# Kernel optimization log

Measured on AMD Instinct MI355X. Metric: run time of the kernel, lower is better.

The kernel has to match this reference:

```python
import math
import jax, jax.numpy as jnp
import numpy as np

T_LEN, BATCH = 215, 256
D_INP = 36; D_MODEL = 36          # d_model must be 36 for internal dims to be consistent
D_T = D_MODEL + 36                # 72: transformer encoder width
N_HEAD = 4; D_HEAD = D_T // N_HEAD
D_FF = 128; N_LAYERS = 2; D_STATIC = 9; N_CLASSES = 2
N_NODES = 36

def _layer_norm(x, g, b, eps=1e-5):
    mu = jnp.mean(x, -1, keepdims=True)
    var = jnp.mean((x - mu) ** 2, -1, keepdims=True)
    return (x - mu) / jnp.sqrt(var + eps) * g + b

def _forward(src, static, times, lengths, W_enc, b_enc, W_emb, b_emb, Wq, bq, Wk, bk, Wv, bv, Wskip, bskip, enc_in_w, enc_in_b, enc_out_w, enc_out_b, enc_ff1_w, enc_ff1_b, enc_ff2_w, enc_ff2_b, enc_ln1_g, enc_ln1_b, enc_ln2_g, enc_ln2_b, mlp_w1, mlp_b1, mlp_w2, mlp_b2):
    T, B = src.shape[0], src.shape[1]
    x = (src[:, :, :D_INP] @ W_enc.T + b_enc) * math.sqrt(D_MODEL)          # [T,B,36]
    # positional encoding: 18 timescales = max_len ** linspace(0,1,18)
    timescales = jnp.asarray(215.0 ** np.linspace(0.0, 1.0, D_MODEL // 2), jnp.float32)
    scaled = times[:, :, None] / timescales                                  # [T,B,18]
    pe = jnp.concatenate([jnp.sin(scaled), jnp.cos(scaled)], -1)             # [T,B,36]
    emb = static @ W_emb.T + b_emb                                           # [B,36]
    mask = jnp.arange(T)[None, :] >= lengths[:, None]                        # [B,T] True = pad
    # --- batched TransformerConv over fully-connected 36-node graph (replaces per-sample loop) ---
    q = x @ Wq.T + bq; k = x @ Wk.T + bk; v = x @ Wv.T + bv
    skip = x @ Wskip.T + bskip
    scores = jnp.einsum('ibe,jbe->bij', q[:N_NODES], k[:N_NODES]) / math.sqrt(36.0)  # i=tgt, j=src
    A = jax.nn.softmax(scores, -1)                      # per-target softmax over incoming edges
    msg = jnp.einsum('bij,jbe->ibe', A, v[:N_NODES])    # edge_weights are all ones
    gout = skip.at[:N_NODES].add(msg)                   # [T,B,36]; rows >= 36 have no in-edges
    # per-edge alpha flattened in nonzero(adj) order: e = src*36 + tgt
    alpha_all = A.transpose(0, 2, 1).reshape(B, N_NODES * N_NODES).T         # [1296,B]
    sq = jnp.sum(alpha_all ** 2, 0)
    d2 = jnp.maximum(sq[:, None] + sq[None, :] - 2.0 * (alpha_all.T @ alpha_all), 0.0)
    distance = jnp.mean(jnp.sqrt(jnp.where(d2 > 0, d2, 1.0)) * (d2 > 0))     # mean pairwise L2
    # --- 2-layer post-norm transformer encoder, width 72, key padding mask ---
    h = jnp.concatenate([gout, pe], -1)                                      # [T,B,72]
    neg = jnp.where(mask[:, None, None, :], -1e9, 0.0)                       # [B,1,1,T]
    for l in range(N_LAYERS):
        qkv = h @ enc_in_w[l].T + enc_in_b[l]
        qh, kh, vh = [t.reshape(T, B, N_HEAD, D_HEAD) for t in jnp.split(qkv, 3, -1)]
        s = jnp.einsum('tbhd,sbhd->bhts', qh, kh) / math.sqrt(D_HEAD) + neg
        ctx = jnp.einsum('bhts,sbhd->tbhd', jax.nn.softmax(s, -1), vh).reshape(T, B, D_T)
        h = _layer_norm(h + ctx @ enc_out_w[l].T + enc_out_b[l], enc_ln1_g[l], enc_ln1_b[l])
        ff = jax.nn.relu(h @ enc_ff1_w[l].T + enc_ff1_b[l]) @ enc_ff2_w[l].T + enc_ff2_b[l]
        h = _layer_norm(h + ff, enc_ln2_g[l], enc_ln2_b[l])
    # masked mean over time, denominator lengths+1 (as in original)
    valid = (~mask).astype(h.dtype).T[:, :, None]                            # [T,B,1]
    pooled = jnp.sum(h * valid, 0) / (lengths.astype(h.dtype)[:, None] + 1.0)
    feat = jnp.concatenate([pooled, emb], -1)                                # [B,108]
    logits = jax.nn.relu(feat @ mlp_w1.T + mlp_b1) @ mlp_w2.T + mlp_b2
    return logits, distance

def setup_inputs() -> dict:
    key = jax.random.key(0)
    ks = jax.random.split(key, 40)
    def nrm(i, shape, s=0.05):
        return jax.random.normal(ks[i], shape, jnp.float32) * s
    return {
        'src': jax.random.normal(ks[0], (T_LEN, BATCH, 2 * D_INP), jnp.float32),
        'static': jax.random.normal(ks[1], (BATCH, D_STATIC), jnp.float32),
        'times': jnp.tile(jnp.arange(T_LEN, dtype=jnp.float32)[:, None], (1, BATCH)),
        'lengths': jax.random.randint(ks[2], (BATCH,), 1, T_LEN + 1),
        'W_enc': nrm(3, (D_MODEL, D_INP)), 'b_enc': jnp.zeros((D_MODEL,), jnp.float32),
        'W_emb': nrm(4, (D_MODEL, D_STATIC)), 'b_emb': jnp.zeros((D_MODEL,), jnp.float32),
        'Wq': nrm(5, (36, 36)), 'bq': nrm(6, (36,)),
        'Wk': nrm(7, (36, 36)), 'bk': nrm(8, (36,)),
        'Wv': nrm(9, (36, 36)), 'bv': nrm(10, (36,)),
        'Wskip': nrm(11, (36, 36)), 'bskip': nrm(12, (36,)),
        'enc_in_w': nrm(13, (N_LAYERS, 3 * D_T, D_T)), 'enc_in_b': nrm(14, (N_LAYERS, 3 * D_T)),
        'enc_out_w': nrm(15, (N_LAYERS, D_T, D_T)), 'enc_out_b': nrm(16, (N_LAYERS, D_T)),
        'enc_ff1_w': nrm(17, (N_LAYERS, D_FF, D_T)), 'enc_ff1_b': nrm(18, (N_LAYERS, D_FF)),
        'enc_ff2_w': nrm(19, (N_LAYERS, D_T, D_FF)), 'enc_ff2_b': nrm(20, (N_LAYERS, D_T)),
        'enc_ln1_g': jnp.ones((N_LAYERS, D_T), jnp.float32), 'enc_ln1_b': jnp.zeros((N_LAYERS, D_T), jnp.float32),
        'enc_ln2_g': jnp.ones((N_LAYERS, D_T), jnp.float32), 'enc_ln2_b': jnp.zeros((N_LAYERS, D_T), jnp.float32),
        'mlp_w1': nrm(21, (108, 108)), 'mlp_b1': nrm(22, (108,)),
        'mlp_w2': nrm(23, (N_CLASSES, 108)), 'mlp_b2': nrm(24, (N_CLASSES,)),
    }

def reference(src, static, times, lengths, W_enc, b_enc, W_emb, b_emb, Wq, bq, Wk, bk, Wv, bv, Wskip, bskip, enc_in_w, enc_in_b, enc_out_w, enc_out_b, enc_ff1_w, enc_ff1_b, enc_ff2_w, enc_ff2_b, enc_ln1_g, enc_ln1_b, enc_ln2_g, enc_ln2_b, mlp_w1, mlp_b1, mlp_w2, mlp_b2):
    return _forward(src, static, times, lengths, W_enc, b_enc, W_emb, b_emb, Wq, bq, Wk, bk, Wv, bv, Wskip, bskip, enc_in_w, enc_in_b, enc_out_w, enc_out_b, enc_ff1_w, enc_ff1_b, enc_ff2_w, enc_ff2_b, enc_ln1_g, enc_ln1_b, enc_ln2_g, enc_ln2_b, mlp_w1, mlp_b1, mlp_w2, mlp_b2)
```

## Files before the change

kernel.cpp:

```cpp
#include <hip/hip_runtime.h>

#define TT 215
#define BB 256
#define ROWS (TT * BB)

typedef __attribute__((ext_vector_type(8))) short short8;
typedef __attribute__((ext_vector_type(4))) float f32x4;

__device__ __forceinline__ unsigned short f2bf_rn(float x) {
    unsigned int u = __float_as_uint(x);
    u = u + 0x7FFFu + ((u >> 16) & 1u);
    return (unsigned short)(u >> 16);
}
__device__ __forceinline__ float bf2f(unsigned short b) {
    return __uint_as_float(((unsigned int)b) << 16);
}

__global__ void k_prep(const float* __restrict__ enc_in_w, const float* __restrict__ ff1_w,
                       const float* __restrict__ ff2_w, const float* __restrict__ enc_out_w,
                       unsigned short* __restrict__ Whi, unsigned short* __restrict__ Wlo,
                       unsigned short* __restrict__ F1hi, unsigned short* __restrict__ F1lo,
                       unsigned short* __restrict__ F2hi, unsigned short* __restrict__ F2lo,
                       unsigned short* __restrict__ Ohi, unsigned short* __restrict__ Olo,
                       float* __restrict__ ts) {
    int g = blockIdx.x * 256 + threadIdx.x;
    if (g < 18) ts[g] = (float)pow(215.0, (double)g / 17.0);
    if (g < 2 * 216 * 96) {
        int l = g / (216 * 96), rem = g % (216 * 96);
        int o = rem / 96, k = rem % 96;
        float v = (k < 72) ? enc_in_w[((size_t)l * 216 + o) * 72 + k] : 0.f;
        unsigned short hi = f2bf_rn(v);
        Whi[g] = hi; Wlo[g] = f2bf_rn(v - bf2f(hi));
    }
    if (g < 2 * 128 * 96) {
        int l = g / (128 * 96), rem = g % (128 * 96);
        int j = rem / 96, k = rem % 96;
        float v = (k < 72) ? ff1_w[((size_t)l * 128 + j) * 72 + k] : 0.f;
        unsigned short hi = f2bf_rn(v);
        F1hi[g] = hi; F1lo[g] = f2bf_rn(v - bf2f(hi));
    }
    if (g < 2 * 72 * 128) {
        float v = ff2_w[g];
        unsigned short hi = f2bf_rn(v);
        F2hi[g] = hi; F2lo[g] = f2bf_rn(v - bf2f(hi));
    }
    if (g < 2 * 72 * 96) {
        int l = g / (72 * 96), rem = g % (72 * 96);
        int o = rem / 96, k = rem % 96;
        float v = (k < 72) ? enc_out_w[((size_t)l * 72 + o) * 72 + k] : 0.f;
        unsigned short hi = f2bf_rn(v);
        Ohi[g] = hi; Olo[g] = f2bf_rn(v - bf2f(hi));
    }
}

__global__ __launch_bounds__(256, 1) void k_enc1(const float* __restrict__ src,
                                                 const float* __restrict__ W,
                                                 const float* __restrict__ bias,
                                                 float* __restrict__ x) {
    int row = blockIdx.x * 256 + threadIdx.x;
    int o0 = blockIdx.y * 9;
    float s[36];
    const float4* sv = (const float4*)(src + (size_t)row * 72);
#pragma unroll
    for (int k = 0; k < 9; ++k) {
        float4 v = sv[k];
        s[4 * k] = v.x; s[4 * k + 1] = v.y; s[4 * k + 2] = v.z; s[4 * k + 3] = v.w;
    }
    float* xp = x + (size_t)row * 36 + o0;
#pragma unroll
    for (int o = 0; o < 9; ++o) {
        float a = bias[o0 + o];
        const float* w = W + (size_t)(o0 + o) * 36;
#pragma unroll
        for (int i = 0; i < 36; ++i) a = fmaf(s[i], w[i], a);
        xp[o] = a * 6.0f;
    }
}

__global__ __launch_bounds__(256, 1) void k_enc2(const float* __restrict__ x,
                                                 const float* __restrict__ W,
                                                 const float* __restrict__ bias,
                                                 float* __restrict__ h) {
    int row = blockIdx.x * 256 + threadIdx.x;
    int o0 = blockIdx.y * 9;
    float xr[36];
    const float4* xv = (const float4*)(x + (size_t)row * 36);
#pragma unroll
    for (int k = 0; k < 9; ++k) {
        float4 v = xv[k];
        xr[4 * k] = v.x; xr[4 * k + 1] = v.y; xr[4 * k + 2] = v.z; xr[4 * k + 3] = v.w;
    }
    float* hp = h + (size_t)row * 72 + o0;
#pragma unroll
    for (int o = 0; o < 9; ++o) {
        float a = bias[o0 + o];
        const float* w = W + (size_t)(o0 + o) * 36;
#pragma unroll
        for (int i = 0; i < 36; ++i) a = fmaf(xr[i], w[i], a);
        hp[o] = a;
    }
}

__global__ __launch_bounds__(256) void k_pe(const float* __restrict__ times,
                                            const float* __restrict__ ts,
                                            float* __restrict__ h) {
    int idx = blockIdx.x * 256 + threadIdx.x;
    int d = idx % 36, row = idx / 36;
    float t = times[row];
    float val;
    if (d < 18) val = sinf(t / ts[d]);
    else        val = cosf(t / ts[d - 18]);
    h[(size_t)row * 72 + 36 + d] = val;
}

__global__ __launch_bounds__(256, 1) void k_graph_qkv(const float* __restrict__ x,
                                                      const float* __restrict__ Wq, const float* __restrict__ bq,
                                                      const float* __restrict__ Wk, const float* __restrict__ bk,
                                                      const float* __restrict__ Wv, const float* __restrict__ bv,
                                                      float* __restrict__ qg, float* __restrict__ kg,
                                                      float* __restrict__ vg) {
    int row = blockIdx.x * 256 + threadIdx.x;
    int mat = blockIdx.y >> 2;
    int o0 = (blockIdx.y & 3) * 9;
    const float* W; const float* bias; float* out;
    if (mat == 0)      { W = Wq; bias = bq; out = qg; }
    else if (mat == 1) { W = Wk; bias = bk; out = kg; }
    else               { W = Wv; bias = bv; out = vg; }
    float xr[36];
    const float4* xv = (const float4*)(x + (size_t)row * 36);
#pragma unroll
    for (int k = 0; k < 9; ++k) {
        float4 v = xv[k];
        xr[4 * k] = v.x; xr[4 * k + 1] = v.y; xr[4 * k + 2] = v.z; xr[4 * k + 3] = v.w;
    }
    float* op = out + (size_t)row * 36 + o0;
#pragma unroll
    for (int o = 0; o < 9; ++o) {
        float a = bias[o0 + o];
        const float* w = W + (size_t)(o0 + o) * 36;
#pragma unroll
        for (int i = 0; i < 36; ++i) a = fmaf(xr[i], w[i], a);
        op[o] = a;
    }
}

__global__ void k_graph_attn(const float* __restrict__ qg, const float* __restrict__ kg,
                             const float* __restrict__ vg, float* __restrict__ h,
                             float* __restrict__ Abuf, float* __restrict__ sqv) {
    __shared__ float q[1296], k[1296], v[1296], A[1296];
    __shared__ float red[128];
    int b = blockIdx.x, tid = threadIdx.x;
    for (int i = tid; i < 1296; i += 128) {
        int t = i / 36, e = i % 36;
        int g = (t * BB + b) * 36 + e;
        q[i] = qg[g]; k[i] = kg[g]; v[i] = vg[g];
    }
    __syncthreads();
    for (int i = tid; i < 1296; i += 128) {
        int r = i / 36, c = i % 36;
        float a = 0.f;
#pragma unroll
        for (int e = 0; e < 36; ++e) a = fmaf(q[r * 36 + e], k[c * 36 + e], a);
        A[i] = a * (1.0f / 6.0f);
    }
    __syncthreads();
    if (tid < 36) {
        float m = -1e30f;
        for (int j = 0; j < 36; ++j) m = fmaxf(m, A[tid * 36 + j]);
        float s = 0.f;
        for (int j = 0; j < 36; ++j) { float e = expf(A[tid * 36 + j] - m); A[tid * 36 + j] = e; s += e; }
        float inv = 1.0f / s;
        for (int j = 0; j < 36; ++j) A[tid * 36 + j] *= inv;
    }
    __syncthreads();
    float lsq = 0.f;
    for (int i = tid; i < 1296; i += 128) {
        float a = A[i];
        Abuf[(size_t)b * 1296 + i] = a;
        lsq = fmaf(a, a, lsq);
        int r = i / 36, e = i % 36;
        float m = 0.f;
#pragma unroll
        for (int j = 0; j < 36; ++j) m = fmaf(A[r * 36 + j], v[j * 36 + e], m);
        h[((size_t)r * BB + b) * 72 + e] += m;
    }
    red[tid] = lsq;
    __syncthreads();
    for (int s = 64; s > 0; s >>= 1) { if (tid < s) red[tid] += red[tid + s]; __syncthreads(); }
    if (tid == 0) sqv[b] = red[0];
}

__global__ void k_gram(const float* __restrict__ Abuf, const float* __restrict__ sqv,
                       float* __restrict__ rowsum) {
    __shared__ float Arow[1296];
    __shared__ float red[256];
    int b1 = blockIdx.x, tid = threadIdx.x;
    for (int i = tid; i < 1296; i += 256) Arow[i] = Abuf[(size_t)b1 * 1296 + i];
    __syncthreads();
    int b2 = tid;
    const float* a2 = Abuf + (size_t)b2 * 1296;
    float dot = 0.f;
    for (int e = 0; e < 1296; ++e) dot = fmaf(Arow[e], a2[e], dot);
    float d2 = fmaxf(sqv[b1] + sqv[b2] - 2.0f * dot, 0.0f);
    red[tid] = (d2 > 0.0f) ? sqrtf(d2) : 0.0f;
    __syncthreads();
    for (int s = 128; s > 0; s >>= 1) { if (tid < s) red[tid] += red[tid + s]; __syncthreads(); }
    if (tid == 0) rowsum[b1] = red[0];
}

__global__ __launch_bounds__(256, 1) void k_qkv(const float* __restrict__ h,
                                                const unsigned short* __restrict__ Whi,
                                                const unsigned short* __restrict__ Wlo,
                                                const float* __restrict__ bias,
                                                float* __restrict__ qkv) {
    int tid = threadIdx.x;
    int w = tid >> 6;
    int lane = tid & 63;
    int n16 = lane & 15;
    int quad = lane >> 4;
    int m0 = blockIdx.x * 64 + w * 16;
    int r = m0 + n16;
    short8 Ahi[3], Alo[3];
#pragma unroll
    for (int s = 0; s < 3; ++s) {
        int k0 = s * 32 + quad * 8;
        float v[8];
        if (k0 < 72) {
            const float4* ap = (const float4*)(h + (size_t)r * 72 + k0);
            float4 v0 = ap[0], v1 = ap[1];
            v[0] = v0.x; v[1] = v0.y; v[2] = v0.z; v[3] = v0.w;
            v[4] = v1.x; v[5] = v1.y; v[6] = v1.z; v[7] = v1.w;
        } else {
#pragma unroll
            for (int j = 0; j < 8; ++j) v[j] = 0.f;
        }
        short8 ph, pl;
#pragma unroll
        for (int j = 0; j < 8; ++j) {
            unsigned short hi = f2bf_rn(v[j]);
            ph[j] = (short)hi;
            pl[j] = (short)f2bf_rn(v[j] - bf2f(hi));
        }
        Ahi[s] = ph; Alo[s] = pl;
    }
    f32x4 acc[14];
#pragma unroll
    for (int t = 0; t < 14; ++t) acc[t] = (f32x4){0.f, 0.f, 0.f, 0.f};
#pragma unroll
    for (int t = 0; t < 14; ++t) {
        int o = t * 16 + n16;
        int oc = (o > 215) ? 215 : o;
        const short8* bh = (const short8*)(Whi + (size_t)oc * 96);
        const short8* bl = (const short8*)(Wlo + (size_t)oc * 96);
        f32x4 a = acc[t];
#pragma unroll
        for (int s = 0; s < 3; ++s) {
            short8 Bh = bh[s * 4 + quad];
            short8 Bl = bl[s * 4 + quad];
            a = __builtin_amdgcn_mfma_f32_16x16x32_bf16(Ahi[s], Bh, a, 0, 0, 0);
            a = __builtin_amdgcn_mfma_f32_16x16x32_bf16(Ahi[s], Bl, a, 0, 0, 0);
            a = __builtin_amdgcn_mfma_f32_16x16x32_bf16(Alo[s], Bh, a, 0, 0, 0);
        }
        acc[t] = a;
    }
#pragma unroll
    for (int t = 0; t < 14; ++t) {
        int col = t * 16 + n16;
        if (col < 216) {
            float b = bias[col];
#pragma unroll
            for (int reg = 0; reg < 4; ++reg) {
                int row = m0 + quad * 4 + reg;
                qkv[(size_t)row * 216 + col] = acc[t][reg] + b;
            }
        }
    }
}

__global__ __launch_bounds__(256, 1) void k_attn(const float* __restrict__ qkv,
                                                 const int* __restrict__ lengths,
                                                 float* __restrict__ ctx) {
    __shared__ __attribute__((aligned(16))) unsigned short Kb[215 * 40];
    __shared__ __attribute__((aligned(16))) unsigned short Vt[32 * 232];
    __shared__ __attribute__((aligned(16))) unsigned short Pw[4][16 * 232];
    int b = blockIdx.x & (BB - 1);
    int hh = blockIdx.x >> 8;
    int tid = threadIdx.x;
    int len = lengths[b];
    for (int i = tid; i < (215 * 40) / 2; i += 256) ((unsigned int*)Kb)[i] = 0u;
    for (int i = tid; i < (32 * 232) / 2; i += 256) ((unsigned int*)Vt)[i] = 0u;
    __syncthreads();
    for (int i = tid; i < len * 18; i += 256) {
        int s = i / 18, d = i % 18;
        size_t base2 = ((size_t)s * BB + b) * 216 + hh * 18 + d;
        Kb[s * 40 + d] = f2bf_rn(qkv[base2 + 72]);
        Vt[d * 232 + s] = f2bf_rn(qkv[base2 + 144]);
    }
    __syncthreads();
    int w = tid >> 6;
    int lane = tid & 63;
    int n16 = lane & 15;
    int quad = lane >> 4;
    const float scale = 0.23570226039551587f;
    int nk2 = (len + 31) >> 5;
    int nkt = nk2 * 2;
    int nstrips = (len + 15) >> 4;
    unsigned short* P = &Pw[w][0];
    for (int strip = w; strip < nstrips; strip += 4) {
        int q0 = strip * 16;
        int qr = q0 + n16; if (qr > 214) qr = 214;
        float qv[8];
#pragma unroll
        for (int j = 0; j < 8; ++j) qv[j] = 0.f;
        {
            const float* qp = qkv + ((size_t)qr * BB + b) * 216 + hh * 18;
            int d0 = quad * 8;
            if (d0 < 16) {
                const float2* q2 = (const float2*)(qp + d0);
                float2 a0 = q2[0], a1 = q2[1], a2 = q2[2], a3 = q2[3];
                qv[0] = a0.x; qv[1] = a0.y; qv[2] = a1.x; qv[3] = a1.y;
                qv[4] = a2.x; qv[5] = a2.y; qv[6] = a3.x; qv[7] = a3.y;
            } else if (d0 == 16) {
                qv[0] = qp[16]; qv[1] = qp[17];
            }
        }
        short8 Qhi, Qlo;
#pragma unroll
        for (int j = 0; j < 8; ++j) {
            float v = qv[j] * scale;
            unsigned short hi = f2bf_rn(v);
            Qhi[j] = (short)hi;
            Qlo[j] = (short)f2bf_rn(v - bf2f(hi));
        }
        float lsum[4] = {0.f, 0.f, 0.f, 0.f};
        for (int kt = 0; kt < nkt; ++kt) {
            int key = kt * 16 + n16;
            int kr = (key > 214) ? 214 : key;
            short8 Bk = *(const short8*)(Kb + kr * 40 + quad * 8);
            f32x4 S = (f32x4){0.f, 0.f, 0.f, 0.f};
            S = __builtin_amdgcn_mfma_f32_16x16x32_bf16(Qlo, Bk, S, 0, 0, 0);
            S = __builtin_amdgcn_mfma_f32_16x16x32_bf16(Qhi, Bk, S, 0, 0, 0);
#pragma unroll
            for (int reg = 0; reg < 4; ++reg) {
                float p = (key < len) ? __expf(S[reg]) : 0.f;
                lsum[reg] += p;
                P[(quad * 4 + reg) * 232 + kt * 16 + n16] = f2bf_rn(p);
            }
        }
#pragma unroll
        for (int m = 1; m < 16; m <<= 1) {
#pragma unroll
            for (int reg = 0; reg < 4; ++reg) lsum[reg] += __shfl_xor(lsum[reg], m);
        }
        f32x4 o0 = (f32x4){0.f, 0.f, 0.f, 0.f};
        f32x4 o1 = (f32x4){0.f, 0.f, 0.f, 0.f};
        for (int k2 = 0; k2 < nk2; ++k2) {
            short8 Af = *(const short8*)(P + n16 * 232 + k2 * 32 + quad * 8);
            short8 Bv0 = *(const short8*)(Vt + n16 * 232 + k2 * 32 + quad * 8);
            short8 Bv1 = *(const short8*)(Vt + (16 + n16) * 232 + k2 * 32 + quad * 8);
            o0 = __builtin_amdgcn_mfma_f32_16x16x32_bf16(Af, Bv0, o0, 0, 0, 0);
            o1 = __builtin_amdgcn_mfma_f32_16x16x32_bf16(Af, Bv1, o1, 0, 0, 0);
        }
#pragma unroll
        for (int reg = 0; reg < 4; ++reg) {
            int t = q0 + quad * 4 + reg;
            if (t < len) {
                float inv = 1.0f / lsum[reg];
                float* cb = ctx + ((size_t)t * BB + b) * 72 + hh * 18;
                cb[n16] = o0[reg] * inv;
                if (n16 < 2) cb[16 + n16] = o1[reg] * inv;
            }
        }
    }
}

__global__ __launch_bounds__(256, 1) void k_outln(const float* __restrict__ ctx,
                                                  const unsigned short* __restrict__ Ohi,
                                                  const unsigned short* __restrict__ Olo,
                                                  const float* __restrict__ bias,
                                                  const float* __restrict__ g,
                                                  const float* __restrict__ beta,
                                                  float* __restrict__ h) {
    int tid = threadIdx.x;
    int w = tid >> 6;
    int lane = tid & 63;
    int n16 = lane & 15;
    int quad = lane >> 4;
    int m0 = blockIdx.x * 64 + w * 16;
    int r = m0 + n16;
    short8 Ahi[3], Alo[3];
#pragma unroll
    for (int s = 0; s < 3; ++s) {
        int k0 = s * 32 + quad * 8;
        float v[8];
        if (k0 < 72) {
            const float4* ap = (const float4*)(ctx + (size_t)r * 72 + k0);
            float4 v0 = ap[0], v1 = ap[1];
            v[0] = v0.x; v[1] = v0.y; v[2] = v0.z; v[3] = v0.w;
            v[4] = v1.x; v[5] = v1.y; v[6] = v1.z; v[7] = v1.w;
        } else {
#pragma unroll
            for (int j = 0; j < 8; ++j) v[j] = 0.f;
        }
        short8 ph, pl;
#pragma unroll
        for (int j = 0; j < 8; ++j) {
            unsigned short hi = f2bf_rn(v[j]);
            ph[j] = (short)hi;
            pl[j] = (short)f2bf_rn(v[j] - bf2f(hi));
        }
        Ahi[s] = ph; Alo[s] = pl;
    }
    f32x4 acc[5];
#pragma unroll
    for (int t = 0; t < 5; ++t) acc[t] = (f32x4){0.f, 0.f, 0.f, 0.f};
#pragma unroll
    for (int t = 0; t < 5; ++t) {
        int o = t * 16 + n16;
        int oc = (o > 71) ? 71 : o;
        const short8* bh = (const short8*)(Ohi + (size_t)oc * 96);
        const short8* bl = (const short8*)(Olo + (size_t)oc * 96);
        f32x4 a = acc[t];
#pragma unroll
        for (int s = 0; s < 3; ++s) {
            short8 Bh = bh[s * 4 + quad];
            short8 Bl = bl[s * 4 + quad];
            a = __builtin_amdgcn_mfma_f32_16x16x32_bf16(Ahi[s], Bh, a, 0, 0, 0);
            a = __builtin_amdgcn_mfma_f32_16x16x32_bf16(Ahi[s], Bl, a, 0, 0, 0);
            a = __builtin_amdgcn_mfma_f32_16x16x32_bf16(Alo[s], Bh, a, 0, 0, 0);
        }
        acc[t] = a;
    }
    float vals[5][4];
#pragma unroll
    for (int t = 0; t < 5; ++t) {
        int o = t * 16 + n16;
        bool valid = (o < 72);
        float bb = valid ? bias[o] : 0.f;
#pragma unroll
        for (int reg = 0; reg < 4; ++reg) {
            int row = m0 + quad * 4 + reg;
            float hv = valid ? h[(size_t)row * 72 + o] : 0.f;
            vals[t][reg] = acc[t][reg] + bb + hv;
        }
    }
#pragma unroll
    for (int reg = 0; reg < 4; ++reg) {
        float s = 0.f, q = 0.f;
#pragma unroll
        for (int t = 0; t < 5; ++t) {
            int o = t * 16 + n16;
            if (o < 72) { s += vals[t][reg]; q = fmaf(vals[t][reg], vals[t][reg], q); }
        }
#pragma unroll
        for (int m = 1; m < 16; m <<= 1) { s += __shfl_xor(s, m); q += __shfl_xor(q, m); }
        float mu = s / 72.0f;
        float var = fmaxf(q / 72.0f - mu * mu, 0.0f);
        float rstd = 1.0f / sqrtf(var + 1e-5f);
        int row = m0 + quad * 4 + reg;
#pragma unroll
        for (int t = 0; t < 5; ++t) {
            int o = t * 16 + n16;
            if (o < 72)
                h[(size_t)row * 72 + o] = (vals[t][reg] - mu) * rstd * g[o] + beta[o];
        }
    }
}

__global__ __launch_bounds__(256, 1) void k_ffln(const unsigned short* __restrict__ F1hi,
                                                 const unsigned short* __restrict__ F1lo,
                                                 const float* __restrict__ b1,
                                                 const unsigned short* __restrict__ F2hi,
                                                 const unsigned short* __restrict__ F2lo,
                                                 const float* __restrict__ b2,
                                                 const float* __restrict__ g,
                                                 const float* __restrict__ beta,
                                                 float* __restrict__ h) {
    __shared__ float hid[64][129];
    int tid = threadIdx.x;
    int w = tid >> 6;
    int lane = tid & 63;
    int n16 = lane & 15;
    int quad = lane >> 4;
    int m0 = blockIdx.x * 64 + w * 16;
    int r = m0 + n16;
    short8 Ahi[3], Alo[3];
#pragma unroll
    for (int s = 0; s < 3; ++s) {
        int k0 = s * 32 + quad * 8;
        float v[8];
        if (k0 < 72) {
            const float4* ap = (const float4*)(h + (size_t)r * 72 + k0);
            float4 v0 = ap[0], v1 = ap[1];
            v[0] = v0.x; v[1] = v0.y; v[2] = v0.z; v[3] = v0.w;
            v[4] = v1.x; v[5] = v1.y; v[6] = v1.z; v[7] = v1.w;
        } else {
#pragma unroll
            for (int j = 0; j < 8; ++j) v[j] = 0.f;
        }
        short8 ph, pl;
#pragma unroll
        for (int j = 0; j < 8; ++j) {
            unsigned short hi = f2bf_rn(v[j]);
            ph[j] = (short)hi;
            pl[j] = (short)f2bf_rn(v[j] - bf2f(hi));
        }
        Ahi[s] = ph; Alo[s] = pl;
    }
#pragma unroll
    for (int t = 0; t < 8; ++t) {
        int j = t * 16 + n16;
        const short8* bh = (const short8*)(F1hi + (size_t)j * 96);
        const short8* bl = (const short8*)(F1lo + (size_t)j * 96);
        f32x4 a = (f32x4){0.f, 0.f, 0.f, 0.f};
#pragma unroll
        for (int s = 0; s < 3; ++s) {
            short8 Bh = bh[s * 4 + quad];
            short8 Bl = bl[s * 4 + quad];
            a = __builtin_amdgcn_mfma_f32_16x16x32_bf16(Ahi[s], Bh, a, 0, 0, 0);
            a = __builtin_amdgcn_mfma_f32_16x16x32_bf16(Ahi[s], Bl, a, 0, 0, 0);
            a = __builtin_amdgcn_mfma_f32_16x16x32_bf16(Alo[s], Bh, a, 0, 0, 0);
        }
        float bb = b1[j];
#pragma unroll
        for (int reg = 0; reg < 4; ++reg)
            hid[w * 16 + quad * 4 + reg][j] = fmaxf(a[reg] + bb, 0.f);
    }
    short8 A2hi[4], A2lo[4];
#pragma unroll
    for (int s = 0; s < 4; ++s) {
        const float* hp = &hid[w * 16 + n16][s * 32 + quad * 8];
        short8 ph, pl;
#pragma unroll
        for (int j = 0; j < 8; ++j) {
            float v = hp[j];
            unsigned short hi = f2bf_rn(v);
            ph[j] = (short)hi;
            pl[j] = (short)f2bf_rn(v - bf2f(hi));
        }
        A2hi[s] = ph; A2lo[s] = pl;
    }
    f32x4 acc[5];
#pragma unroll
    for (int t = 0; t < 5; ++t) acc[t] = (f32x4){0.f, 0.f, 0.f, 0.f};
#pragma unroll
    for (int t = 0; t < 5; ++t) {
        int o = t * 16 + n16;
        int oc = (o > 71) ? 71 : o;
        const short8* bh = (const short8*)(F2hi + (size_t)oc * 128);
        const short8* bl = (const short8*)(F2lo + (size_t)oc * 128);
        f32x4 a = acc[t];
#pragma unroll
        for (int s = 0; s < 4; ++s) {
            short8 Bh = bh[s * 4 + quad];
            short8 Bl = bl[s * 4 + quad];
            a = __builtin_amdgcn_mfma_f32_16x16x32_bf16(A2hi[s], Bh, a, 0, 0, 0);
            a = __builtin_amdgcn_mfma_f32_16x16x32_bf16(A2hi[s], Bl, a, 0, 0, 0);
            a = __builtin_amdgcn_mfma_f32_16x16x32_bf16(A2lo[s], Bh, a, 0, 0, 0);
        }
        acc[t] = a;
    }
    float vals[5][4];
#pragma unroll
    for (int t = 0; t < 5; ++t) {
        int o = t * 16 + n16;
        bool valid = (o < 72);
        float bb = valid ? b2[o] : 0.f;
#pragma unroll
        for (int reg = 0; reg < 4; ++reg) {
            int row = m0 + quad * 4 + reg;
            float hv = valid ? h[(size_t)row * 72 + o] : 0.f;
            vals[t][reg] = acc[t][reg] + bb + hv;
        }
    }
#pragma unroll
    for (int reg = 0; reg < 4; ++reg) {
        float s = 0.f, q = 0.f;
#pragma unroll
        for (int t = 0; t < 5; ++t) {
            int o = t * 16 + n16;
            if (o < 72) { s += vals[t][reg]; q = fmaf(vals[t][reg], vals[t][reg], q); }
        }
#pragma unroll
        for (int m = 1; m < 16; m <<= 1) { s += __shfl_xor(s, m); q += __shfl_xor(q, m); }
        float mu = s / 72.0f;
        float var = fmaxf(q / 72.0f - mu * mu, 0.0f);
        float rstd = 1.0f / sqrtf(var + 1e-5f);
        int row = m0 + quad * 4 + reg;
#pragma unroll
        for (int t = 0; t < 5; ++t) {
            int o = t * 16 + n16;
            if (o < 72)
                h[(size_t)row * 72 + o] = (vals[t][reg] - mu) * rstd * g[o] + beta[o];
        }
    }
}

__global__ void k_head(const float* __restrict__ h, const int* __restrict__ lengths,
                       const float* __restrict__ statics, const float* __restrict__ W_emb,
                       const float* __restrict__ b_emb, const float* __restrict__ w1,
                       const float* __restrict__ bb1, const float* __restrict__ w2,
                       const float* __restrict__ bb2, float* __restrict__ out) {
    __shared__ float ps2[4][72];
    __shared__ float feat[108];
    __shared__ float hidm[108];
    __shared__ float st[9];
    int b = blockIdx.x, tid = threadIdx.x;
    int w = tid >> 6, lane = tid & 63;
    int len = lengths[b];
    if (tid < 9) st[tid] = statics[b * 9 + tid];
    for (int idx = tid; idx < 288; idx += 256) ((float*)ps2)[idx] = 0.f;
    __syncthreads();
#pragma unroll
    for (int c0 = 0; c0 < 128; c0 += 64) {
        int col = c0 + lane;
        if (col < 72) {
            float s = 0.f;
            for (int t = w; t < len; t += 4) s += h[((size_t)t * BB + b) * 72 + col];
            ps2[w][col] = s;
        }
    }
    __syncthreads();
    if (tid < 72)
        feat[tid] = (ps2[0][tid] + ps2[1][tid] + ps2[2][tid] + ps2[3][tid]) / ((float)len + 1.0f);
    if (tid >= 128 && tid < 164) {
        int o = tid - 128;
        float a = b_emb[o];
#pragma unroll
        for (int i = 0; i < 9; ++i) a = fmaf(st[i], W_emb[o * 9 + i], a);
        feat[72 + o] = a;
    }
    __syncthreads();
    if (tid < 108) {
        float a = bb1[tid];
        for (int i = 0; i < 108; ++i) a = fmaf(feat[i], w1[tid * 108 + i], a);
        hidm[tid] = fmaxf(a, 0.f);
    }
    __syncthreads();
    if (tid < 2) {
        float a = bb2[tid];
        for (int i = 0; i < 108; ++i) a = fmaf(hidm[i], w2[tid * 108 + i], a);
        out[b * 2 + tid] = a;
    }
}

__global__ void k_dist(const float* __restrict__ rowsum, float* __restrict__ out) {
    __shared__ float red[256];
    int tid = threadIdx.x;
    red[tid] = rowsum[tid];
    __syncthreads();
    for (int s = 128; s > 0; s >>= 1) { if (tid < s) red[tid] += red[tid + s]; __syncthreads(); }
    if (tid == 0) out[2 * BB] = red[0] / 65536.0f;
}

extern "C" void kernel_launch(void* const* d_in, const int* in_sizes, int n_in,
                              void* d_out, int out_size, void* d_ws, size_t ws_size,
                              hipStream_t stream) {
    const float* src     = (const float*)d_in[0];
    const float* statics = (const float*)d_in[1];
    const float* times   = (const float*)d_in[2];
    const int*   lengths = (const int*)d_in[3];
    const float* W_enc = (const float*)d_in[4];  const float* b_enc = (const float*)d_in[5];
    const float* W_emb = (const float*)d_in[6];  const float* b_emb = (const float*)d_in[7];
    const float* Wq = (const float*)d_in[8];     const float* bq = (const float*)d_in[9];
    const float* Wk = (const float*)d_in[10];    const float* bk = (const float*)d_in[11];
    const float* Wv = (const float*)d_in[12];    const float* bv = (const float*)d_in[13];
    const float* Wskip = (const float*)d_in[14]; const float* bskip = (const float*)d_in[15];
    const float* enc_in_w = (const float*)d_in[16];  const float* enc_in_b = (const float*)d_in[17];
    const float* enc_out_w = (const float*)d_in[18]; const float* enc_out_b = (const float*)d_in[19];
    const float* ff1_w = (const float*)d_in[20]; const float* ff1_b = (const float*)d_in[21];
    const float* ff2_w = (const float*)d_in[22]; const float* ff2_b = (const float*)d_in[23];
    const float* ln1_g = (const float*)d_in[24]; const float* ln1_b = (const float*)d_in[25];
    const float* ln2_g = (const float*)d_in[26]; const float* ln2_b = (const float*)d_in[27];
    const float* w1 = (const float*)d_in[28];    const float* bb1 = (const float*)d_in[29];
    const float* w2 = (const float*)d_in[30];    const float* bb2 = (const float*)d_in[31];
    float* out = (float*)d_out;

    float* p = (float*)d_ws;
    float* x    = p; p += (size_t)ROWS * 36;
    float* h    = p; p += (size_t)ROWS * 72;
    float* qkv  = p; p += (size_t)ROWS * 216;
    float* ctx  = p; p += (size_t)ROWS * 72;
    float* qg   = p; p += (size_t)36 * BB * 36;
    float* kg   = p; p += (size_t)36 * BB * 36;
    float* vg   = p; p += (size_t)36 * BB * 36;
    float* Abuf = p; p += (size_t)BB * 1296;
    float* sqv  = p; p += BB;
    float* rsum = p; p += BB;
    float* ts   = p; p += 32;
    unsigned short* Whi  = (unsigned short*)p; p += (2 * 216 * 96) / 2;
    unsigned short* Wlo  = (unsigned short*)p; p += (2 * 216 * 96) / 2;
    unsigned short* F1hi = (unsigned short*)p; p += (2 * 128 * 96) / 2;
    unsigned short* F1lo = (unsigned short*)p; p += (2 * 128 * 96) / 2;
    unsigned short* F2hi = (unsigned short*)p; p += (2 * 72 * 128) / 2;
    unsigned short* F2lo = (unsigned short*)p; p += (2 * 72 * 128) / 2;
    unsigned short* Ohi  = (unsigned short*)p; p += (2 * 72 * 96) / 2;
    unsigned short* Olo  = (unsigned short*)p; p += (2 * 72 * 96) / 2;

    k_prep<<<162, 256, 0, stream>>>(enc_in_w, ff1_w, ff2_w, enc_out_w,
                                    Whi, Wlo, F1hi, F1lo, F2hi, F2lo, Ohi, Olo, ts);
    k_enc1<<<dim3(TT, 4), 256, 0, stream>>>(src, W_enc, b_enc, x);
    k_enc2<<<dim3(TT, 4), 256, 0, stream>>>(x, Wskip, bskip, h);
    k_pe<<<(ROWS * 36) / 256, 256, 0, stream>>>(times, ts, h);
    k_graph_qkv<<<dim3(36, 12), 256, 0, stream>>>(x, Wq, bq, Wk, bk, Wv, bv, qg, kg, vg);
    k_graph_attn<<<BB, 128, 0, stream>>>(qg, kg, vg, h, Abuf, sqv);
    k_gram<<<BB, 256, 0, stream>>>(Abuf, sqv, rsum);
    for (int l = 0; l < 2; ++l) {
        k_qkv<<<ROWS / 64, 256, 0, stream>>>(h, Whi + (size_t)l * 216 * 96,
                                             Wlo + (size_t)l * 216 * 96,
                                             enc_in_b + l * 216, qkv);
        k_attn<<<BB * 4, 256, 0, stream>>>(qkv, lengths, ctx);
        k_outln<<<ROWS / 64, 256, 0, stream>>>(ctx, Ohi + (size_t)l * 72 * 96,
                                               Olo + (size_t)l * 72 * 96, enc_out_b + l * 72,
                                               ln1_g + l * 72, ln1_b + l * 72, h);
        k_ffln<<<ROWS / 64, 256, 0, stream>>>(F1hi + (size_t)l * 128 * 96,
                                              F1lo + (size_t)l * 128 * 96, ff1_b + l * 128,
                                              F2hi + (size_t)l * 72 * 128,
                                              F2lo + (size_t)l * 72 * 128, ff2_b + l * 72,
                                              ln2_g + l * 72, ln2_b + l * 72, h);
    }
    k_head<<<BB, 256, 0, stream>>>(h, lengths, statics, W_emb, b_emb, w1, bb1, w2, bb2, out);
    k_dist<<<1, 256, 0, stream>>>(rsum, out);
}
```

Baseline: 500.3 us.

## Compute graph-attention Gram matrix with split-bf16 MFMA tiles

The 256x256 Gram matrix of flattened attention maps was computed with scalar FMAs, one thread per column pair, each reading 1296 floats straight from global memory. The attention kernel now stores each map as hi/lo bf16 pairs padded to 1312 entries, and k_gram computes 32x32 tiles with 16x16x32 bf16 MFMA in three-term split precision. Each block reduces its sqrt-distance partial sum and writes it to a 64-entry buffer that k_dist sums. The split-bf16 dot product drops the lo*lo term, so results differ slightly from fp32.

```diff
diff --git a/kernel.cpp b/kernel.cpp
--- a/kernel.cpp
+++ b/kernel.cpp
@@ -146,7 +146,8 @@
 
 __global__ void k_graph_attn(const float* __restrict__ qg, const float* __restrict__ kg,
                              const float* __restrict__ vg, float* __restrict__ h,
-                             float* __restrict__ Abuf, float* __restrict__ sqv) {
+                             unsigned short* __restrict__ Ahi, unsigned short* __restrict__ Alo,
+                             float* __restrict__ sqv) {
     __shared__ float q[1296], k[1296], v[1296], A[1296];
     __shared__ float red[128];
     int b = blockIdx.x, tid = threadIdx.x;
@@ -176,7 +177,9 @@
     float lsq = 0.f;
     for (int i = tid; i < 1296; i += 128) {
         float a = A[i];
-        Abuf[(size_t)b * 1296 + i] = a;
+        unsigned short hi = f2bf_rn(a);
+        Ahi[(size_t)b * 1312 + i] = hi;
+        Alo[(size_t)b * 1312 + i] = f2bf_rn(a - bf2f(hi));
         lsq = fmaf(a, a, lsq);
         int r = i / 36, e = i % 36;
         float m = 0.f;
@@ -184,28 +187,54 @@
         for (int j = 0; j < 36; ++j) m = fmaf(A[r * 36 + j], v[j * 36 + e], m);
         h[((size_t)r * BB + b) * 72 + e] += m;
     }
+    if (tid < 16) {
+        Ahi[(size_t)b * 1312 + 1296 + tid] = 0;
+        Alo[(size_t)b * 1312 + 1296 + tid] = 0;
+    }
     red[tid] = lsq;
     __syncthreads();
     for (int s = 64; s > 0; s >>= 1) { if (tid < s) red[tid] += red[tid + s]; __syncthreads(); }
     if (tid == 0) sqv[b] = red[0];
 }
 
-__global__ void k_gram(const float* __restrict__ Abuf, const float* __restrict__ sqv,
-                       float* __restrict__ rowsum) {
-    __shared__ float Arow[1296];
-    __shared__ float red[256];
-    int b1 = blockIdx.x, tid = threadIdx.x;
-    for (int i = tid; i < 1296; i += 256) Arow[i] = Abuf[(size_t)b1 * 1296 + i];
-    __syncthreads();
-    int b2 = tid;
-    const float* a2 = Abuf + (size_t)b2 * 1296;
-    float dot = 0.f;
-    for (int e = 0; e < 1296; ++e) dot = fmaf(Arow[e], a2[e], dot);
-    float d2 = fmaxf(sqv[b1] + sqv[b2] - 2.0f * dot, 0.0f);
-    red[tid] = (d2 > 0.0f) ? sqrtf(d2) : 0.0f;
-    __syncthreads();
-    for (int s = 128; s > 0; s >>= 1) { if (tid < s) red[tid] += red[tid + s]; __syncthreads(); }
-    if (tid == 0) rowsum[b1] = red[0];
+__global__ __launch_bounds__(256, 1) void k_gram(const unsigned short* __restrict__ Ahi,
+                                                 const unsigned short* __restrict__ Alo,
+                                                 const float* __restrict__ sqv,
+                                                 float* __restrict__ bpart) {
+    __shared__ float red[4];
+    int tid = threadIdx.x;
+    int w = tid >> 6;
+    int lane = tid & 63;
+    int n16 = lane & 15;
+    int quad = lane >> 4;
+    int i0 = (blockIdx.x >> 3) * 32 + (w >> 1) * 16;
+    int j0 = (blockIdx.x & 7) * 32 + (w & 1) * 16;
+    const short8* Ari = (const short8*)(Ahi + (size_t)(i0 + n16) * 1312);
+    const short8* Arl = (const short8*)(Alo + (size_t)(i0 + n16) * 1312);
+    const short8* Bri = (const short8*)(Ahi + (size_t)(j0 + n16) * 1312);
+    const short8* Brl = (const short8*)(Alo + (size_t)(j0 + n16) * 1312);
+    f32x4 acc = (f32x4){0.f, 0.f, 0.f, 0.f};
+    for (int k2 = 0; k2 < 41; ++k2) {
+        int ko = k2 * 4 + quad;
+        short8 ah = Ari[ko], al = Arl[ko];
+        short8 bh = Bri[ko], bl = Brl[ko];
+        acc = __builtin_amdgcn_mfma_f32_16x16x32_bf16(ah, bh, acc, 0, 0, 0);
+        acc = __builtin_amdgcn_mfma_f32_16x16x32_bf16(ah, bl, acc, 0, 0, 0);
+        acc = __builtin_amdgcn_mfma_f32_16x16x32_bf16(al, bh, acc, 0, 0, 0);
+    }
+    float part = 0.f;
+#pragma unroll
+    for (int reg = 0; reg < 4; ++reg) {
+        int i = i0 + quad * 4 + reg;
+        int j = j0 + n16;
+        float d2 = fmaxf(sqv[i] + sqv[j] - 2.0f * acc[reg], 0.0f);
+        part += (d2 > 0.0f) ? sqrtf(d2) : 0.0f;
+    }
+#pragma unroll
+    for (int m = 1; m < 64; m <<= 1) part += __shfl_xor(part, m);
+    if (lane == 0) red[w] = part;
+    __syncthreads();
+    if (tid == 0) bpart[blockIdx.x] = red[0] + red[1] + red[2] + red[3];
 }
 
 __global__ __launch_bounds__(256, 1) void k_qkv(const float* __restrict__ h,
@@ -644,12 +673,12 @@
     }
 }
 
-__global__ void k_dist(const float* __restrict__ rowsum, float* __restrict__ out) {
-    __shared__ float red[256];
+__global__ void k_dist(const float* __restrict__ bpart, float* __restrict__ out) {
+    __shared__ float red[64];
     int tid = threadIdx.x;
-    red[tid] = rowsum[tid];
-    __syncthreads();
-    for (int s = 128; s > 0; s >>= 1) { if (tid < s) red[tid] += red[tid + s]; __syncthreads(); }
+    red[tid] = bpart[tid];
+    __syncthreads();
+    for (int s = 32; s > 0; s >>= 1) { if (tid < s) red[tid] += red[tid + s]; __syncthreads(); }
     if (tid == 0) out[2 * BB] = red[0] / 65536.0f;
 }
 
@@ -684,10 +713,11 @@
     float* qg   = p; p += (size_t)36 * BB * 36;
     float* kg   = p; p += (size_t)36 * BB * 36;
     float* vg   = p; p += (size_t)36 * BB * 36;
-    float* Abuf = p; p += (size_t)BB * 1296;
     float* sqv  = p; p += BB;
-    float* rsum = p; p += BB;
+    float* bpart = p; p += 64;
     float* ts   = p; p += 32;
+    unsigned short* GAhi = (unsigned short*)p; p += (BB * 1312) / 2;
+    unsigned short* GAlo = (unsigned short*)p; p += (BB * 1312) / 2;
     unsigned short* Whi  = (unsigned short*)p; p += (2 * 216 * 96) / 2;
     unsigned short* Wlo  = (unsigned short*)p; p += (2 * 216 * 96) / 2;
     unsigned short* F1hi = (unsigned short*)p; p += (2 * 128 * 96) / 2;
@@ -703,8 +733,8 @@
     k_enc2<<<dim3(TT, 4), 256, 0, stream>>>(x, Wskip, bskip, h);
     k_pe<<<(ROWS * 36) / 256, 256, 0, stream>>>(times, ts, h);
     k_graph_qkv<<<dim3(36, 12), 256, 0, stream>>>(x, Wq, bq, Wk, bk, Wv, bv, qg, kg, vg);
-    k_graph_attn<<<BB, 128, 0, stream>>>(qg, kg, vg, h, Abuf, sqv);
-    k_gram<<<BB, 256, 0, stream>>>(Abuf, sqv, rsum);
+    k_graph_attn<<<BB, 128, 0, stream>>>(qg, kg, vg, h, GAhi, GAlo, sqv);
+    k_gram<<<64, 256, 0, stream>>>(GAhi, GAlo, sqv, bpart);
     for (int l = 0; l < 2; ++l) {
         k_qkv<<<ROWS / 64, 256, 0, stream>>>(h, Whi + (size_t)l * 216 * 96,
                                              Wlo + (size_t)l * 216 * 96,
@@ -720,5 +750,5 @@
                                               ln2_g + l * 72, ln2_b + l * 72, h);
     }
     k_head<<<BB, 256, 0, stream>>>(h, lengths, statics, W_emb, b_emb, w1, bb1, w2, bb2, out);
-    k_dist<<<1, 256, 0, stream>>>(rsum, out);
-}
+    k_dist<<<1, 64, 0, stream>>>(bpart, out);
+}
```

After: 474.0 us. 5.3% less time.
